# Kernel optimization log

Hardware: AMD Instinct MI355X
Metric: run time of the kernel (lower is better)

Reference implementation:

```python
import jax, jax.numpy as jnp
import numpy as np

ALPHA = 0.05
GDEP = 3
HID = 20  # self.hidden_num in the torch module


def setup_inputs() -> dict:
    key = jax.random.key(0)
    ks = jax.random.split(key, 6)
    B, C_IN, N, C = 8, 32, 1024, 16
    C_OUT = 32
    x = jax.random.normal(ks[0], (B, C_IN, N, C), dtype=jnp.float32)
    adj = jax.random.uniform(ks[1], (B, C, N, N), dtype=jnp.float32)
    W_start = jax.random.normal(ks[2], (C_IN, HID), dtype=jnp.float32) / np.sqrt(C_IN)
    b_start = jax.random.normal(ks[3], (HID,), dtype=jnp.float32) * 0.01
    W_end = jax.random.normal(ks[4], (HID * (GDEP + 1), C_OUT), dtype=jnp.float32) / np.sqrt(HID * (GDEP + 1))
    b_end = jax.random.normal(ks[5], (C_OUT,), dtype=jnp.float32) * 0.01
    return {"x": x, "adj": adj, "W_start": W_start, "b_start": b_start,
            "W_end": W_end, "b_end": b_end}


def reference(x, adj, W_start, b_start, W_end, b_end):
    # x: [B, c_in, N, C]; adj: [B, C, N, N]
    N = adj.shape[-1]
    # vectorized degree normalization: A_hat = (A + I) / rowsum(A + I)
    A = adj + jnp.eye(N, dtype=adj.dtype)
    A = A / A.sum(axis=-1, keepdims=True)
    # transpose(1,3) then mlp_start -> h0: [B, C, N, HID]
    xt = jnp.transpose(x, (0, 3, 2, 1))
    h0 = jnp.einsum('bcni,ih->bcnh', xt, W_start) + b_start
    h = h0
    outs = [h0]
    for _ in range(GDEP):
        # torch einsum 'ncwl,ncvw->ncvl' == A[b,c,v,w] @ h[b,c,w,l]
        h = ALPHA * h0 + (1.0 - ALPHA) * jnp.einsum('bcvw,bcwh->bcvh', A, h)
        outs.append(h)
    ho = jnp.concatenate(outs, axis=-1)  # [B, C, N, HID*(GDEP+1)]
    return jnp.einsum('bcnk,ko->bcno', ho, W_end) + b_end
```

## Files before the change

kernel.cpp:

```cpp
#include <hip/hip_runtime.h>
#include <stdint.h>

#define ALPHA 0.05f
constexpr int B_   = 8;
constexpr int CIN  = 32;
constexpr int NN   = 1024;
constexpr int CC   = 16;
constexpr int HID_ = 20;
constexpr int COUT = 32;
constexpr int PAIRS = B_ * CC;

typedef __attribute__((ext_vector_type(8))) short bf8;
typedef __attribute__((ext_vector_type(4))) float f4;

__device__ inline unsigned short f2bf(float x) {
    union { float f; uint32_t u; } v; v.f = x;
    uint32_t u = v.u;
    u += 0x7fffu + ((u >> 16) & 1u);
    return (unsigned short)(u >> 16);
}

constexpr int CSTR = 268;

__global__ __launch_bounds__(256) void k_conv(const float* __restrict__ adj,
                                              unsigned short* __restrict__ Asw) {
    int pair = blockIdx.y;
    int rb = blockIdx.x >> 2;
    int cb = blockIdx.x & 3;
    __shared__ unsigned short T[64 * CSTR];
    int t = threadIdx.x;

    const float* src = adj + ((size_t)pair * NN + rb * 64) * NN + cb * 256;
    #pragma unroll
    for (int j = 0; j < 16; j++) {
        int idx = j * 256 + t;
        int row = idx >> 6, c4 = idx & 63;
        float4 v = *(const float4*)(src + (size_t)row * NN + c4 * 4);
        ushort4 w;
        w.x = f2bf(v.x); w.y = f2bf(v.y); w.z = f2bf(v.z); w.w = f2bf(v.w);
        *(ushort4*)&T[row * CSTR + c4 * 4] = w;
    }
    __syncthreads();

    int lane = t & 63, wave = t >> 6;
    int ml = lane & 15, quad = lane >> 4;
    unsigned short* dst = Asw +
        (((size_t)pair * 64 + rb * 4 + wave) * 32 + cb * 8) * 512 + lane * 8;
    const unsigned short* srcT = &T[(wave * 16 + ml) * CSTR + quad * 8];
    #pragma unroll
    for (int kb = 0; kb < 8; kb++) {
        uint2 lo = *(const uint2*)(srcT + kb * 32);
        uint2 hi = *(const uint2*)(srcT + kb * 32 + 4);
        uint4 o; o.x = lo.x; o.y = lo.y; o.z = hi.x; o.w = hi.y;
        *(uint4*)(dst + (size_t)kb * 512) = o;
    }
}

__global__ __launch_bounds__(256) void k_h0(const float* __restrict__ x,
                                            const float* __restrict__ Ws,
                                            const float* __restrict__ bs,
                                            float* __restrict__ h0) {
    int b = blockIdx.y, n0 = blockIdx.x * 16;
    __shared__ float xs[CIN * 16 * CC];
    __shared__ float WsS[CIN * HID_];
    __shared__ float bsS[HID_];
    int t = threadIdx.x;

    #pragma unroll
    for (int j = 0; j < 8; j++) {
        int idx = t + j * 256;
        int i = idx >> 6, f = idx & 63;
        ((float4*)xs)[idx] =
            ((const float4*)(x + ((size_t)(b * CIN + i) * NN + n0) * CC))[f];
    }
    for (int j = t; j < CIN * HID_; j += 256) WsS[j] = Ws[j];
    if (t < HID_) bsS[t] = bs[t];
    __syncthreads();

    int c = t & 15, nl = t >> 4;
    float acc[HID_];
    #pragma unroll
    for (int l = 0; l < HID_; l++) acc[l] = bsS[l];
    for (int i = 0; i < CIN; i++) {
        float xv = xs[i * 256 + nl * 16 + c];
        #pragma unroll
        for (int l = 0; l < HID_; l++) acc[l] += xv * WsS[i * HID_ + l];
    }
    float* dst = h0 + ((size_t)(b * CC + c) * NN + (n0 + nl)) * HID_;
    #pragma unroll
    for (int l = 0; l < HID_; l++) dst[l] = acc[l];
}

constexpr int BSTR = 1032;

__global__ __launch_bounds__(512, 4) void k_prop(
        const unsigned short* __restrict__ Asw,
        const float* __restrict__ h_in,
        const float* __restrict__ h0,
        float* __restrict__ h_out) {
    int pair = blockIdx.y;
    int m0 = blockIdx.x * 256;
    __shared__ unsigned short Ht[32 * BSTR];
    int t = threadIdx.x;
    int lane = t & 63, wave = t >> 6;
    int ml = lane & 15, quad = lane >> 4;

    const float* hp = h_in + (size_t)pair * NN * HID_;
    for (int k = t; k < NN; k += 512) {
        float4 v0 = *(const float4*)(hp + (size_t)k * HID_ + 0);
        float4 v1 = *(const float4*)(hp + (size_t)k * HID_ + 4);
        float4 v2 = *(const float4*)(hp + (size_t)k * HID_ + 8);
        float4 v3 = *(const float4*)(hp + (size_t)k * HID_ + 12);
        float4 v4 = *(const float4*)(hp + (size_t)k * HID_ + 16);
        float vv[20] = {v0.x, v0.y, v0.z, v0.w, v1.x, v1.y, v1.z, v1.w,
                        v2.x, v2.y, v2.z, v2.w, v3.x, v3.y, v3.z, v3.w,
                        v4.x, v4.y, v4.z, v4.w};
        #pragma unroll
        for (int l = 0; l < HID_; l++) Ht[l * BSTR + k] = f2bf(vv[l]);
    }
    {
        uint4 ones; ones.x = ones.y = ones.z = ones.w = 0x3F803F80u;
        uint4 zero; zero.x = zero.y = zero.z = zero.w = 0u;
        for (int idx = t; idx < 12 * (NN / 8); idx += 512) {
            int row = 20 + (idx >> 7), seg = idx & 127;
            *(uint4*)&Ht[row * BSTR + seg * 8] = (row == 20) ? ones : zero;
        }
    }
    __syncthreads();

    f4 acc[2][2];
    #pragma unroll
    for (int mt = 0; mt < 2; mt++)
        #pragma unroll
        for (int nt = 0; nt < 2; nt++)
            #pragma unroll
            for (int r = 0; r < 4; r++) acc[mt][nt][r] = 0.0f;

    const unsigned short* At0 = Asw +
        ((size_t)pair * 64 + blockIdx.x * 16 + wave * 2) * (32 * 512) + lane * 8;
    const unsigned short* At1 = At0 + 32 * 512;
    const int b0off = ml * BSTR + quad * 8;
    const int b1off = b0off + 16 * BSTR;

    bf8 cA0 = *(const bf8*)(At0);
    bf8 cA1 = *(const bf8*)(At1);
    bf8 cB0 = *(const bf8*)(At0 + 512);
    bf8 cB1 = *(const bf8*)(At1 + 512);

    #pragma unroll 1
    for (int ks = 0; ks < NN; ks += 64) {
        int kb = ks >> 5;
        int kn = (kb + 2 < 32) ? (kb + 2) : 0;
        bf8 nA0 = *(const bf8*)(At0 + kn * 512);
        bf8 nA1 = *(const bf8*)(At1 + kn * 512);
        bf8 nB0 = *(const bf8*)(At0 + kn * 512 + 512);
        bf8 nB1 = *(const bf8*)(At1 + kn * 512 + 512);
        {
            bf8 b0 = *(const bf8*)&Ht[b0off + ks];
            bf8 b1 = *(const bf8*)&Ht[b1off + ks];
            acc[0][0] = __builtin_amdgcn_mfma_f32_16x16x32_bf16(cA0, b0, acc[0][0], 0, 0, 0);
            acc[0][1] = __builtin_amdgcn_mfma_f32_16x16x32_bf16(cA0, b1, acc[0][1], 0, 0, 0);
            acc[1][0] = __builtin_amdgcn_mfma_f32_16x16x32_bf16(cA1, b0, acc[1][0], 0, 0, 0);
            acc[1][1] = __builtin_amdgcn_mfma_f32_16x16x32_bf16(cA1, b1, acc[1][1], 0, 0, 0);
        }
        {
            bf8 b0 = *(const bf8*)&Ht[b0off + ks + 32];
            bf8 b1 = *(const bf8*)&Ht[b1off + ks + 32];
            acc[0][0] = __builtin_amdgcn_mfma_f32_16x16x32_bf16(cB0, b0, acc[0][0], 0, 0, 0);
            acc[0][1] = __builtin_amdgcn_mfma_f32_16x16x32_bf16(cB0, b1, acc[0][1], 0, 0, 0);
            acc[1][0] = __builtin_amdgcn_mfma_f32_16x16x32_bf16(cB1, b0, acc[1][0], 0, 0, 0);
            acc[1][1] = __builtin_amdgcn_mfma_f32_16x16x32_bf16(cB1, b1, acc[1][1], 0, 0, 0);
        }
        cA0 = nA0; cA1 = nA1; cB0 = nB0; cB1 = nB1;
    }

    #pragma unroll
    for (int mt = 0; mt < 2; mt++) {
        #pragma unroll
        for (int r = 0; r < 4; r++) {
            int row = m0 + wave * 32 + mt * 16 + quad * 4 + r;
            float s = __shfl(acc[mt][1][r], (quad << 4) + 4, 64) + 1.0f;
            float inv_s = (1.0f - ALPHA) / s;
            {
                size_t off = ((size_t)pair * NN + row) * HID_ + ml;
                h_out[off] = ALPHA * h0[off] + inv_s * (acc[mt][0][r] + h_in[off]);
            }
            if (ml < 4) {
                size_t off = ((size_t)pair * NN + row) * HID_ + 16 + ml;
                h_out[off] = ALPHA * h0[off] + inv_s * (acc[mt][1][r] + h_in[off]);
            }
        }
    }
}

__global__ __launch_bounds__(256) void k_out(const float* __restrict__ h0,
                                             const float* __restrict__ h1,
                                             const float* __restrict__ h2,
                                             const float* __restrict__ h3,
                                             const float* __restrict__ We,
                                             const float* __restrict__ be,
                                             float* __restrict__ out) {
    int pair = blockIdx.y, n0 = blockIdx.x * 128;
    int t = threadIdx.x;
    __shared__ float WeT[32 * 84];
    __shared__ float beS[32];
    for (int idx = t; idx < 80 * 32; idx += 256) {
        int k = idx >> 5, o = idx & 31;
        WeT[o * 84 + k] = We[idx];
    }
    if (t < 32) beS[t] = be[t];
    __syncthreads();

    const float* hs[4] = {h0, h1, h2, h3};
    int og = t & 7, ng = t >> 3;
    float acc[4][4];
    #pragma unroll
    for (int r = 0; r < 4; r++)
        #pragma unroll
        for (int c = 0; c < 4; c++) acc[r][c] = beS[og + c * 8];

    #pragma unroll
    for (int src = 0; src < 4; src++) {
        const float* hp = hs[src] + ((size_t)pair * NN + n0 + ng) * HID_;
        #pragma unroll
        for (int j = 0; j < 5; j++) {
            float4 hv[4];
            #pragma unroll
            for (int r = 0; r < 4; r++)
                hv[r] = *(const float4*)(hp + (size_t)(r * 32) * HID_ + j * 4);
            #pragma unroll
            for (int c = 0; c < 4; c++) {
                float4 wv = *(const float4*)&WeT[(og + c * 8) * 84 + src * 20 + j * 4];
                #pragma unroll
                for (int r = 0; r < 4; r++)
                    acc[r][c] += hv[r].x * wv.x + hv[r].y * wv.y +
                                 hv[r].z * wv.z + hv[r].w * wv.w;
            }
        }
    }
    #pragma unroll
    for (int r = 0; r < 4; r++)
        #pragma unroll
        for (int c = 0; c < 4; c++)
            out[((size_t)pair * NN + n0 + ng + r * 32) * COUT + og + c * 8] = acc[r][c];
}

extern "C" void kernel_launch(void* const* d_in, const int* in_sizes, int n_in,
                              void* d_out, int out_size, void* d_ws, size_t ws_size,
                              hipStream_t stream) {
    const float* x   = (const float*)d_in[0];
    const float* adj = (const float*)d_in[1];
    const float* Ws  = (const float*)d_in[2];
    const float* bs  = (const float*)d_in[3];
    const float* We  = (const float*)d_in[4];
    const float* be  = (const float*)d_in[5];
    float* out = (float*)d_out;

    const size_t HSZ = (size_t)PAIRS * NN * HID_;
    float* h0 = (float*)d_ws;
    float* h1 = h0 + HSZ;
    float* h2 = h1 + HSZ;
    float* h3 = h2 + HSZ;
    unsigned short* Asw = (unsigned short*)(h3 + HSZ);

    k_conv<<<dim3(64, PAIRS), 256, 0, stream>>>(adj, Asw);
    k_h0  <<<dim3(64, 8),     256, 0, stream>>>(x, Ws, bs, h0);
    k_prop<<<dim3(4, PAIRS),  512, 0, stream>>>(Asw, h0, h0, h1);
    k_prop<<<dim3(4, PAIRS),  512, 0, stream>>>(Asw, h1, h0, h2);
    k_prop<<<dim3(4, PAIRS),  512, 0, stream>>>(Asw, h2, h0, h3);
    k_out <<<dim3(8, PAIRS),  256, 0, stream>>>(h0, h1, h2, h3, We, be, out);
}
```

Before: 957.6 us.

## Fuse adjacency bf16 conversion into first propagation step

Removes the separate conversion kernel. The first propagation kernel now reads fp32 adj directly, converts it to bf16 through a per-wave LDS tile, feeds it to the MFMAs, and writes the swizzled bf16 copy out for the later propagation steps. This saves one full read of adj plus a kernel launch. It also shrinks the shared H tile from 32 to 21 rows by clamping the second B-tile row index, which cuts LDS use and drops the zero-fill. The risk is that the fused kernel now carries the fp32 load latency inside the MFMA loop with no prefetch.

```diff
diff --git a/kernel.cpp b/kernel.cpp
--- a/kernel.cpp
+++ b/kernel.cpp
@@ -20,41 +20,9 @@
     return (unsigned short)(u >> 16);
 }
 
-constexpr int CSTR = 268;
-
-__global__ __launch_bounds__(256) void k_conv(const float* __restrict__ adj,
-                                              unsigned short* __restrict__ Asw) {
-    int pair = blockIdx.y;
-    int rb = blockIdx.x >> 2;
-    int cb = blockIdx.x & 3;
-    __shared__ unsigned short T[64 * CSTR];
-    int t = threadIdx.x;
-
-    const float* src = adj + ((size_t)pair * NN + rb * 64) * NN + cb * 256;
-    #pragma unroll
-    for (int j = 0; j < 16; j++) {
-        int idx = j * 256 + t;
-        int row = idx >> 6, c4 = idx & 63;
-        float4 v = *(const float4*)(src + (size_t)row * NN + c4 * 4);
-        ushort4 w;
-        w.x = f2bf(v.x); w.y = f2bf(v.y); w.z = f2bf(v.z); w.w = f2bf(v.w);
-        *(ushort4*)&T[row * CSTR + c4 * 4] = w;
-    }
-    __syncthreads();
-
-    int lane = t & 63, wave = t >> 6;
-    int ml = lane & 15, quad = lane >> 4;
-    unsigned short* dst = Asw +
-        (((size_t)pair * 64 + rb * 4 + wave) * 32 + cb * 8) * 512 + lane * 8;
-    const unsigned short* srcT = &T[(wave * 16 + ml) * CSTR + quad * 8];
-    #pragma unroll
-    for (int kb = 0; kb < 8; kb++) {
-        uint2 lo = *(const uint2*)(srcT + kb * 32);
-        uint2 hi = *(const uint2*)(srcT + kb * 32 + 4);
-        uint4 o; o.x = lo.x; o.y = lo.y; o.z = hi.x; o.w = hi.y;
-        *(uint4*)(dst + (size_t)kb * 512) = o;
-    }
-}
+constexpr int BSTR = 1032;
+constexpr int HTR  = 21;
+constexpr int ATS  = 72;
 
 __global__ __launch_bounds__(256) void k_h0(const float* __restrict__ x,
                                             const float* __restrict__ Ws,
@@ -91,7 +59,101 @@
     for (int l = 0; l < HID_; l++) dst[l] = acc[l];
 }
 
-constexpr int BSTR = 1032;
+__global__ __launch_bounds__(512, 4) void k_prop1f(
+        const float* __restrict__ adj,
+        const float* __restrict__ h0g,
+        float* __restrict__ h_out,
+        unsigned short* __restrict__ Asw) {
+    int pair = blockIdx.y, bx = blockIdx.x;
+    int m0 = bx * 256;
+    __shared__ unsigned short Ht[HTR * BSTR];
+    __shared__ unsigned short Atr[8][32 * ATS];
+    int t = threadIdx.x;
+    int lane = t & 63, wave = t >> 6;
+    int ml = lane & 15, quad = lane >> 4;
+
+    const float* hp = h0g + (size_t)pair * NN * HID_;
+    for (int k = t; k < NN; k += 512) {
+        float4 v0 = *(const float4*)(hp + (size_t)k * HID_ + 0);
+        float4 v1 = *(const float4*)(hp + (size_t)k * HID_ + 4);
+        float4 v2 = *(const float4*)(hp + (size_t)k * HID_ + 8);
+        float4 v3 = *(const float4*)(hp + (size_t)k * HID_ + 12);
+        float4 v4 = *(const float4*)(hp + (size_t)k * HID_ + 16);
+        float vv[20] = {v0.x, v0.y, v0.z, v0.w, v1.x, v1.y, v1.z, v1.w,
+                        v2.x, v2.y, v2.z, v2.w, v3.x, v3.y, v3.z, v3.w,
+                        v4.x, v4.y, v4.z, v4.w};
+        #pragma unroll
+        for (int l = 0; l < HID_; l++) Ht[l * BSTR + k] = f2bf(vv[l]);
+    }
+    {
+        uint4 ones; ones.x = ones.y = ones.z = ones.w = 0x3F803F80u;
+        for (int idx = t; idx < NN / 8; idx += 512)
+            *(uint4*)&Ht[20 * BSTR + idx * 8] = ones;
+    }
+    __syncthreads();
+
+    f4 acc[2][2];
+    #pragma unroll
+    for (int mt = 0; mt < 2; mt++)
+        #pragma unroll
+        for (int nt = 0; nt < 2; nt++)
+            #pragma unroll
+            for (int r = 0; r < 4; r++) acc[mt][nt][r] = 0.0f;
+
+    const float* ap = adj + ((size_t)pair * NN + m0 + wave * 32) * NN;
+    unsigned short* AtrW = &Atr[wave][0];
+    const int b0off = ml * BSTR + quad * 8;
+    const int b1off = ((16 + ml <= 20) ? (16 + ml) : 20) * BSTR + quad * 8;
+    unsigned short* aswp = Asw +
+        ((size_t)pair * 64 + bx * 16 + wave * 2) * (32 * 512) + lane * 8;
+
+    #pragma unroll 1
+    for (int ks = 0; ks < NN; ks += 64) {
+        float4 v[8];
+        #pragma unroll
+        for (int q = 0; q < 8; q++)
+            v[q] = *(const float4*)(ap + (size_t)(q * 4 + quad) * NN + ks + ml * 4);
+        #pragma unroll
+        for (int q = 0; q < 8; q++) {
+            ushort4 w;
+            w.x = f2bf(v[q].x); w.y = f2bf(v[q].y);
+            w.z = f2bf(v[q].z); w.w = f2bf(v[q].w);
+            *(ushort4*)&AtrW[(q * 4 + quad) * ATS + ml * 4] = w;
+        }
+        #pragma unroll
+        for (int kb = 0; kb < 2; kb++) {
+            bf8 b0 = *(const bf8*)&Ht[b0off + ks + kb * 32];
+            bf8 b1 = *(const bf8*)&Ht[b1off + ks + kb * 32];
+            #pragma unroll
+            for (int mt = 0; mt < 2; mt++) {
+                bf8 a = *(const bf8*)&AtrW[(mt * 16 + ml) * ATS + kb * 32 + quad * 8];
+                acc[mt][0] = __builtin_amdgcn_mfma_f32_16x16x32_bf16(a, b0, acc[mt][0], 0, 0, 0);
+                acc[mt][1] = __builtin_amdgcn_mfma_f32_16x16x32_bf16(a, b1, acc[mt][1], 0, 0, 0);
+                *(bf8*)(aswp + (size_t)(mt * 32 + (ks >> 5) + kb) * 512) = a;
+            }
+        }
+    }
+
+    #pragma unroll
+    for (int mt = 0; mt < 2; mt++) {
+        #pragma unroll
+        for (int r = 0; r < 4; r++) {
+            int row = m0 + wave * 32 + mt * 16 + quad * 4 + r;
+            float s = __shfl(acc[mt][1][r], (quad << 4) + 4, 64) + 1.0f;
+            float inv_s = (1.0f - ALPHA) / s;
+            {
+                size_t off = ((size_t)pair * NN + row) * HID_ + ml;
+                float h0v = h0g[off];
+                h_out[off] = ALPHA * h0v + inv_s * (acc[mt][0][r] + h0v);
+            }
+            if (ml < 4) {
+                size_t off = ((size_t)pair * NN + row) * HID_ + 16 + ml;
+                float h0v = h0g[off];
+                h_out[off] = ALPHA * h0v + inv_s * (acc[mt][1][r] + h0v);
+            }
+        }
+    }
+}
 
 __global__ __launch_bounds__(512, 4) void k_prop(
         const unsigned short* __restrict__ Asw,
@@ -100,7 +162,7 @@
         float* __restrict__ h_out) {
     int pair = blockIdx.y;
     int m0 = blockIdx.x * 256;
-    __shared__ unsigned short Ht[32 * BSTR];
+    __shared__ unsigned short Ht[HTR * BSTR];
     int t = threadIdx.x;
     int lane = t & 63, wave = t >> 6;
     int ml = lane & 15, quad = lane >> 4;
@@ -120,11 +182,8 @@
     }
     {
         uint4 ones; ones.x = ones.y = ones.z = ones.w = 0x3F803F80u;
-        uint4 zero; zero.x = zero.y = zero.z = zero.w = 0u;
-        for (int idx = t; idx < 12 * (NN / 8); idx += 512) {
-            int row = 20 + (idx >> 7), seg = idx & 127;
-            *(uint4*)&Ht[row * BSTR + seg * 8] = (row == 20) ? ones : zero;
-        }
+        for (int idx = t; idx < NN / 8; idx += 512)
+            *(uint4*)&Ht[20 * BSTR + idx * 8] = ones;
     }
     __syncthreads();
 
@@ -140,7 +199,7 @@
         ((size_t)pair * 64 + blockIdx.x * 16 + wave * 2) * (32 * 512) + lane * 8;
     const unsigned short* At1 = At0 + 32 * 512;
     const int b0off = ml * BSTR + quad * 8;
-    const int b1off = b0off + 16 * BSTR;
+    const int b1off = ((16 + ml <= 20) ? (16 + ml) : 20) * BSTR + quad * 8;
 
     bf8 cA0 = *(const bf8*)(At0);
     bf8 cA1 = *(const bf8*)(At1);
@@ -263,10 +322,9 @@
     float* h3 = h2 + HSZ;
     unsigned short* Asw = (unsigned short*)(h3 + HSZ);
 
-    k_conv<<<dim3(64, PAIRS), 256, 0, stream>>>(adj, Asw);
-    k_h0  <<<dim3(64, 8),     256, 0, stream>>>(x, Ws, bs, h0);
-    k_prop<<<dim3(4, PAIRS),  512, 0, stream>>>(Asw, h0, h0, h1);
-    k_prop<<<dim3(4, PAIRS),  512, 0, stream>>>(Asw, h1, h0, h2);
-    k_prop<<<dim3(4, PAIRS),  512, 0, stream>>>(Asw, h2, h0, h3);
-    k_out <<<dim3(8, PAIRS),  256, 0, stream>>>(h0, h1, h2, h3, We, be, out);
-}
+    k_h0    <<<dim3(64, 8),    256, 0, stream>>>(x, Ws, bs, h0);
+    k_prop1f<<<dim3(4, PAIRS), 512, 0, stream>>>(adj, h0, h1, Asw);
+    k_prop  <<<dim3(4, PAIRS), 512, 0, stream>>>(Asw, h1, h0, h2);
+    k_prop  <<<dim3(4, PAIRS), 512, 0, stream>>>(Asw, h2, h0, h3);
+    k_out   <<<dim3(8, PAIRS), 256, 0, stream>>>(h0, h1, h2, h3, We, be, out);
+}
```

New measurement: 951.4 us. About the same (-0.6%).
